# Performance work log

Hardware: AMD Instinct MI355X
Metric: run time of the kernel (lower is better)

The kernel has to match this reference:

```python
import jax, jax.numpy as jnp
import numpy as np

B, S, I, H, N_ODE = 256, 64, 256, 1024, 4


def setup_inputs() -> dict:
    key = jax.random.key(0)
    ks = jax.random.split(key, 6)
    x = jax.random.normal(ks[0], (B, S, I), dtype=jnp.float32)
    t = jnp.arange(S, dtype=jnp.float32) * 0.1  # increasing observation times
    W_in = jax.random.normal(ks[1], (H, I), dtype=jnp.float32) / np.float32(np.sqrt(I))
    b_in = jnp.zeros((H,), dtype=jnp.float32)
    W_h = jax.random.normal(ks[2], (H, H), dtype=jnp.float32) / np.float32(np.sqrt(H))
    b_h = jnp.zeros((H,), dtype=jnp.float32)
    W_ode = jax.random.normal(ks[3], (H, H), dtype=jnp.float32) / np.float32(np.sqrt(H))
    b_ode = jnp.zeros((H,), dtype=jnp.float32)
    return {"x": x, "t": t, "W_in": W_in, "b_in": b_in, "W_h": W_h,
            "b_h": b_h, "W_ode": W_ode, "b_ode": b_ode}


def reference(x, t, W_in, b_in, W_h, b_h, W_ode, b_ode):
    # x: [B, S, I], t: [S]. ODE-RNN: per timestep, evolve h by N_ODE Euler
    # steps of dh/dt = tanh(W_ode h + b_ode) over [t_{i-1}, t_i], then
    # h = tanh(W_in x_i + b_in + W_h h + b_h). First step has dt = 0
    # (original uses t[i] for both endpoints when i == 0).
    t_prev = jnp.concatenate([t[:1], t[:-1]])
    dts = t - t_prev  # [S]

    def step(h, inp):
        x_i, dt = inp  # x_i: [B, I], dt: scalar
        dth = dt / N_ODE
        def euler(hc, _):
            return hc + dth * jnp.tanh(hc @ W_ode.T + b_ode), None
        h, _ = jax.lax.scan(euler, h, None, length=N_ODE)
        h = jnp.tanh(x_i @ W_in.T + b_in + h @ W_h.T + b_h)
        return h, None

    h0 = jnp.zeros((x.shape[0], W_h.shape[0]), dtype=x.dtype)
    xs = jnp.swapaxes(x, 0, 1)  # [S, B, I]
    h_final, _ = jax.lax.scan(step, h0, (xs, dts))
    return h_final  # [B, H]
```

## Files before the change

### kernel.cpp

```cpp
#include <hip/hip_runtime.h>

#define B_ 256
#define S_ 64
#define I_ 256
#define H_ 1024
#define NODE_ 4
#define NB 256
#define NG 8
#define GSZ 32

typedef __attribute__((ext_vector_type(8))) short short8;
typedef __attribute__((ext_vector_type(4))) float f32x4;

__device__ __forceinline__ short f2bf(float f) {
    unsigned u = __float_as_uint(f);
    u += 0x7fffu + ((u >> 16) & 1u);
    return (short)(u >> 16);
}
__device__ __forceinline__ unsigned pack2(float a, float b) {
    return (unsigned)(unsigned short)f2bf(a) | ((unsigned)(unsigned short)f2bf(b) << 16);
}

__device__ __forceinline__ float ftanh(float x) {
    float e = __expf(2.0f * fabsf(x));
    float r = __builtin_fmaf(-2.0f, __builtin_amdgcn_rcpf(e + 1.0f), 1.0f);
    return copysignf(r, x);
}

__device__ __forceinline__ void gbar(unsigned* cnt, unsigned target) {
    __syncthreads();
    if (threadIdx.x == 0) {
        __hip_atomic_fetch_add(cnt, 1u, __ATOMIC_RELAXED, __HIP_MEMORY_SCOPE_AGENT);
        while (__hip_atomic_load(cnt, __ATOMIC_RELAXED, __HIP_MEMORY_SCOPE_AGENT) < target)
            __builtin_amdgcn_s_sleep(1);
    }
    __syncthreads();
}

__global__ __launch_bounds__(256, 1)
void odernn_persist(const float* __restrict__ x, const float* __restrict__ t,
                    const float* __restrict__ W_in, const float* __restrict__ b_in,
                    const float* __restrict__ W_h, const float* __restrict__ b_h,
                    const float* __restrict__ W_ode, const float* __restrict__ b_ode,
                    float* __restrict__ out,
                    unsigned short* __restrict__ h0buf, unsigned short* __restrict__ h1buf,
                    unsigned short* __restrict__ Whbf, unsigned short* __restrict__ Winbf,
                    unsigned* __restrict__ cnts)
{
    __shared__ short Wlds[32 * 1024];
    __shared__ short Hlds[32 * 1024];

    const int tid = threadIdx.x;
    const int blk = blockIdx.x;
    const int bi = blk & 7;
    const int bj = blk >> 3;
    const int lane = tid & 63;
    const int wv = tid >> 6;
    const int wr = wv >> 1, wc = wv & 1;
    const int r16 = lane & 15, kg = lane >> 4;

    {
        const int g = blk * 256 + tid;
        const float* src = W_h + (size_t)g * 16;
        unsigned* dst = (unsigned*)Whbf + (size_t)g * 8;
#pragma unroll
        for (int i = 0; i < 4; ++i) {
            float4 v = *(const float4*)(src + i * 4);
            __hip_atomic_store(dst + i * 2,     pack2(v.x, v.y), __ATOMIC_RELAXED, __HIP_MEMORY_SCOPE_AGENT);
            __hip_atomic_store(dst + i * 2 + 1, pack2(v.z, v.w), __ATOMIC_RELAXED, __HIP_MEMORY_SCOPE_AGENT);
        }
        float4 v = *(const float4*)(W_in + (size_t)g * 4);
        unsigned* d2 = (unsigned*)Winbf + (size_t)g * 2;
        __hip_atomic_store(d2,     pack2(v.x, v.y), __ATOMIC_RELAXED, __HIP_MEMORY_SCOPE_AGENT);
        __hip_atomic_store(d2 + 1, pack2(v.z, v.w), __ATOMIC_RELAXED, __HIP_MEMORY_SCOPE_AGENT);
    }

    {
        const int c = tid >> 3;
        const int ks = (tid & 7) * 128;
        const float* wsrc = W_ode + (size_t)(bj * 32 + c) * H_ + ks;
        for (int i = 0; i < 16; ++i) {
            float4 v0 = *(const float4*)(wsrc + i * 8);
            float4 v1 = *(const float4*)(wsrc + i * 8 + 4);
            short8 sv = { f2bf(v0.x), f2bf(v0.y), f2bf(v0.z), f2bf(v0.w),
                          f2bf(v1.x), f2bf(v1.y), f2bf(v1.z), f2bf(v1.w) };
            int idx = c * 1024 + ks + i * 8;
            *(short8*)&Wlds[idx ^ ((c & 7) << 3)] = sv;
        }
    }

    const int rowb = bi * 32 + wr * 16 + kg * 4;
    const int arow = bi * 32 + wr * 16 + r16;
    const int col  = bj * 32 + wc * 16 + r16;
    const int wb   = wc * 16 + r16;

    const int hrow = wr * 16 + r16;
    const char* aBase = (const char*)Hlds + hrow * 2048;
    const int hswz = (hrow & 7) << 4;

    const float bodec = b_ode[col];
    const float binc  = b_in[col] + b_h[col];

    f32x4 hreg = {0.f, 0.f, 0.f, 0.f};
#pragma unroll
    for (int r = 0; r < 4; ++r)
        __hip_atomic_store(&h0buf[(size_t)(rowb + r) * H_ + col], (unsigned short)0,
                           __ATOMIC_RELAXED, __HIP_MEMORY_SCOPE_AGENT);

    gbar(cnts + NG * 64, NB);

    unsigned* gc = cnts + bi * 64;
    unsigned tar = GSZ;

    const unsigned short* hin = h0buf;
    unsigned short* hout = h1buf;

    auto stage = [&](const unsigned short* hsrc) {
        const unsigned long long* src =
            (const unsigned long long*)(hsrc + (size_t)bi * 32 * H_);
        unsigned long long v[32];
#pragma unroll
        for (int i = 0; i < 32; ++i)
            v[i] = __hip_atomic_load(src + i * 256 + tid,
                                     __ATOMIC_RELAXED, __HIP_MEMORY_SCOPE_AGENT);
#pragma unroll
        for (int i = 0; i < 32; ++i) {
            int byte = i * 2048 + (((tid * 8) & 2047) ^ ((i & 7) << 4));
            *(unsigned long long*)((char*)Hlds + byte) = v[i];
        }
        __syncthreads();
    };

    for (int s = 0; s < S_; ++s) {
        if (s > 0) {
            const float dth = (t[s] - t[s - 1]) * 0.25f;
            for (int e = 0; e < NODE_; ++e) {
                stage(hin);
                f32x4 acc = {0.f, 0.f, 0.f, 0.f};
#pragma unroll
                for (int k0 = 0; k0 < H_; k0 += 32) {
                    short8 a = *(const short8*)(aBase + (((k0 + kg * 8) * 2) ^ hswz));
                    short8 b = *(const short8*)&Wlds[(wb * 1024 + k0 + kg * 8) ^ ((wb & 7) << 3)];
                    acc = __builtin_amdgcn_mfma_f32_16x16x32_bf16(a, b, acc, 0, 0, 0);
                }
#pragma unroll
                for (int r = 0; r < 4; ++r) {
                    hreg[r] += dth * ftanh(acc[r] + bodec);
                    __hip_atomic_store(&hout[(size_t)(rowb + r) * H_ + col],
                                       (unsigned short)f2bf(hreg[r]),
                                       __ATOMIC_RELAXED, __HIP_MEMORY_SCOPE_AGENT);
                }
                gbar(gc, tar); tar += GSZ;
                const unsigned short* tmp = hin; hin = hout; hout = (unsigned short*)tmp;
            }
        }
        {
            stage(hin);
            f32x4 acc = {0.f, 0.f, 0.f, 0.f};
            const unsigned short* whB = Whbf + (size_t)col * H_ + kg * 8;
#pragma unroll 8
            for (int k0 = 0; k0 < H_; k0 += 32) {
                short8 a = *(const short8*)(aBase + (((k0 + kg * 8) * 2) ^ hswz));
                short8 b = *(const short8*)(whB + k0);
                acc = __builtin_amdgcn_mfma_f32_16x16x32_bf16(a, b, acc, 0, 0, 0);
            }
            const float* xB = x + ((size_t)arow * S_ + s) * I_ + kg * 8;
            const unsigned short* wiB = Winbf + (size_t)col * I_ + kg * 8;
#pragma unroll
            for (int k2 = 0; k2 < I_; k2 += 32) {
                float4 a0 = *(const float4*)(xB + k2);
                float4 a1 = *(const float4*)(xB + k2 + 4);
                short8 a = { f2bf(a0.x), f2bf(a0.y), f2bf(a0.z), f2bf(a0.w),
                             f2bf(a1.x), f2bf(a1.y), f2bf(a1.z), f2bf(a1.w) };
                short8 b = *(const short8*)(wiB + k2);
                acc = __builtin_amdgcn_mfma_f32_16x16x32_bf16(a, b, acc, 0, 0, 0);
            }
            const bool last = (s == S_ - 1);
#pragma unroll
            for (int r = 0; r < 4; ++r) {
                float v = ftanh(acc[r] + binc);
                hreg[r] = v;
                if (last) {
                    out[(size_t)(rowb + r) * H_ + col] = v;
                } else {
                    __hip_atomic_store(&hout[(size_t)(rowb + r) * H_ + col],
                                       (unsigned short)f2bf(v),
                                       __ATOMIC_RELAXED, __HIP_MEMORY_SCOPE_AGENT);
                }
            }
            if (!last) {
                gbar(gc, tar); tar += GSZ;
                const unsigned short* tmp = hin; hin = hout; hout = (unsigned short*)tmp;
            }
        }
    }
}

extern "C" void kernel_launch(void* const* d_in, const int* in_sizes, int n_in,
                              void* d_out, int out_size, void* d_ws, size_t ws_size,
                              hipStream_t stream) {
    const float* x     = (const float*)d_in[0];
    const float* t     = (const float*)d_in[1];
    const float* W_in  = (const float*)d_in[2];
    const float* b_in  = (const float*)d_in[3];
    const float* W_h   = (const float*)d_in[4];
    const float* b_h   = (const float*)d_in[5];
    const float* W_ode = (const float*)d_in[6];
    const float* b_ode = (const float*)d_in[7];

    unsigned short* h0    = (unsigned short*)d_ws;
    unsigned short* h1    = h0 + (size_t)B_ * H_;
    unsigned short* Whbf  = h1 + (size_t)B_ * H_;
    unsigned short* Winbf = Whbf + (size_t)H_ * H_;
    unsigned* cnts = (unsigned*)(Winbf + (size_t)H_ * I_);

    (void)hipMemsetAsync(cnts, 0, (NG * 64 + 1) * sizeof(unsigned), stream);

    odernn_persist<<<dim3(NB), dim3(256), 0, stream>>>(
        x, t, W_in, b_in, W_h, b_h, W_ode, b_ode,
        (float*)d_out, h0, h1, Whbf, Winbf, cnts);
}
```

Before: 1.345 ms.

## Use XCC-local barriers and coalesced plain loads when a group shares an XCD

Each block reads its XCC id from a hardware register and records per-group min and max ids. When every block in a group runs on the same XCD, the group uses a device-local (non-coherent-scope) atomic counter polled with buffer_inv, plain vectorized 16-byte loads for staging h, and plain stores. Publishing h now goes through LDS so each thread writes contiguous 8-byte chunks instead of scattered 2-byte atomic stores. This aims to cut the cross-die coherence and latency cost of the per-step group barrier and h exchange, but it relies on XCD placement and L2-local atomics behaving as assumed, and it adds extra syncthreads per step.

```diff
diff --git a/kernel.cpp b/kernel.cpp
--- a/kernel.cpp
+++ b/kernel.cpp
@@ -27,12 +27,48 @@
     return copysignf(r, x);
 }
 
-__device__ __forceinline__ void gbar(unsigned* cnt, unsigned target) {
+__device__ __forceinline__ unsigned get_xcc() {
+    unsigned x;
+    asm volatile("s_getreg_b32 %0, hwreg(20, 0, 32)" : "=s"(x));
+    return x & 0xfu;
+}
+
+__device__ __forceinline__ void gbar_slow(unsigned* cnt, unsigned target) {
     __syncthreads();
     if (threadIdx.x == 0) {
         __hip_atomic_fetch_add(cnt, 1u, __ATOMIC_RELAXED, __HIP_MEMORY_SCOPE_AGENT);
         while (__hip_atomic_load(cnt, __ATOMIC_RELAXED, __HIP_MEMORY_SCOPE_AGENT) < target)
             __builtin_amdgcn_s_sleep(1);
+    }
+    __syncthreads();
+}
+
+__device__ __forceinline__ void gbar2(unsigned* gcl, unsigned* gca, unsigned target, bool fast) {
+    __syncthreads();
+    if (threadIdx.x == 0) {
+        if (fast) {
+            unsigned one = 1;
+            asm volatile("global_atomic_add %0, %1, off" :: "v"(gcl), "v"(one) : "memory");
+            __hip_atomic_fetch_add(gca, 1u, __ATOMIC_RELAXED, __HIP_MEMORY_SCOPE_AGENT);
+            unsigned v; unsigned it = 0;
+            for (;;) {
+                asm volatile("buffer_inv\n\t"
+                             "s_waitcnt vmcnt(0)\n\t"
+                             "global_load_dword %0, %1, off\n\t"
+                             "s_waitcnt vmcnt(0)"
+                             : "=&v"(v) : "v"(gcl) : "memory");
+                if (v >= target) break;
+                if ((++it & 15u) == 0 &&
+                    __hip_atomic_load(gca, __ATOMIC_RELAXED, __HIP_MEMORY_SCOPE_AGENT) >= target)
+                    break;
+                __builtin_amdgcn_s_sleep(1);
+            }
+            asm volatile("buffer_inv\n\ts_waitcnt vmcnt(0)" ::: "memory");
+        } else {
+            __hip_atomic_fetch_add(gca, 1u, __ATOMIC_RELAXED, __HIP_MEMORY_SCOPE_AGENT);
+            while (__hip_atomic_load(gca, __ATOMIC_RELAXED, __HIP_MEMORY_SCOPE_AGENT) < target)
+                __builtin_amdgcn_s_sleep(1);
+        }
     }
     __syncthreads();
 }
@@ -88,6 +124,24 @@
             *(short8*)&Wlds[idx ^ ((c & 7) << 3)] = sv;
         }
     }
+    __syncthreads();
+
+    if (tid == 0) {
+        asm volatile("buffer_inv sc1\n\ts_waitcnt vmcnt(0)" ::: "memory");
+        unsigned xc = get_xcc();
+        __hip_atomic_fetch_max(&cnts[516 + bi], xc, __ATOMIC_RELAXED, __HIP_MEMORY_SCOPE_AGENT);
+        __hip_atomic_fetch_max(&cnts[524],      xc, __ATOMIC_RELAXED, __HIP_MEMORY_SCOPE_AGENT);
+        __hip_atomic_fetch_min(&cnts[525 + bi], xc, __ATOMIC_RELAXED, __HIP_MEMORY_SCOPE_AGENT);
+        __hip_atomic_fetch_min(&cnts[533],      xc, __ATOMIC_RELAXED, __HIP_MEMORY_SCOPE_AGENT);
+    }
+
+    gbar_slow(&cnts[512], NB);
+
+    const bool fast =
+        (__hip_atomic_load(&cnts[524], __ATOMIC_RELAXED, __HIP_MEMORY_SCOPE_AGENT) !=
+         __hip_atomic_load(&cnts[533], __ATOMIC_RELAXED, __HIP_MEMORY_SCOPE_AGENT)) &&
+        (__hip_atomic_load(&cnts[516 + bi], __ATOMIC_RELAXED, __HIP_MEMORY_SCOPE_AGENT) ==
+         __hip_atomic_load(&cnts[525 + bi], __ATOMIC_RELAXED, __HIP_MEMORY_SCOPE_AGENT));
 
     const int rowb = bi * 32 + wr * 16 + kg * 4;
     const int arow = bi * 32 + wr * 16 + r16;
@@ -107,28 +161,55 @@
         __hip_atomic_store(&h0buf[(size_t)(rowb + r) * H_ + col], (unsigned short)0,
                            __ATOMIC_RELAXED, __HIP_MEMORY_SCOPE_AGENT);
 
-    gbar(cnts + NG * 64, NB);
-
-    unsigned* gc = cnts + bi * 64;
+    unsigned* gca = cnts + bi * 64;
+    unsigned* gcl = cnts + bi * 64 + 32;
     unsigned tar = GSZ;
+
+    gbar2(gcl, gca, tar, fast); tar += GSZ;
 
     const unsigned short* hin = h0buf;
     unsigned short* hout = h1buf;
 
     auto stage = [&](const unsigned short* hsrc) {
-        const unsigned long long* src =
-            (const unsigned long long*)(hsrc + (size_t)bi * 32 * H_);
-        unsigned long long v[32];
-#pragma unroll
-        for (int i = 0; i < 32; ++i)
-            v[i] = __hip_atomic_load(src + i * 256 + tid,
-                                     __ATOMIC_RELAXED, __HIP_MEMORY_SCOPE_AGENT);
-#pragma unroll
-        for (int i = 0; i < 32; ++i) {
-            int byte = i * 2048 + (((tid * 8) & 2047) ^ ((i & 7) << 4));
-            *(unsigned long long*)((char*)Hlds + byte) = v[i];
+        if (fast) {
+            const char* sp = (const char*)(hsrc + (size_t)bi * 32 * H_);
+#pragma unroll
+            for (int i = 0; i < 16; ++i) {
+                f32x4 v = *(const f32x4*)(sp + i * 4096 + tid * 16);
+                int off = i * 4096 + tid * 16;
+                int row = off >> 11, c = off & 2047;
+                *(f32x4*)((char*)Hlds + row * 2048 + (c ^ ((row & 7) << 4))) = v;
+            }
+        } else {
+            const unsigned long long* src =
+                (const unsigned long long*)(hsrc + (size_t)bi * 32 * H_);
+            unsigned long long v[32];
+#pragma unroll
+            for (int i = 0; i < 32; ++i)
+                v[i] = __hip_atomic_load(src + i * 256 + tid,
+                                         __ATOMIC_RELAXED, __HIP_MEMORY_SCOPE_AGENT);
+#pragma unroll
+            for (int i = 0; i < 32; ++i) {
+                int byte = i * 2048 + (((tid * 8) & 2047) ^ ((i & 7) << 4));
+                *(unsigned long long*)((char*)Hlds + byte) = v[i];
+            }
         }
         __syncthreads();
+    };
+
+    auto publish = [&](unsigned short* dst, f32x4 pv) {
+        __syncthreads();
+        short* Hp = (short*)Hlds;
+#pragma unroll
+        for (int r = 0; r < 4; ++r)
+            Hp[(wr * 16 + kg * 4 + r) * 32 + wc * 16 + r16] = f2bf(pv[r]);
+        __syncthreads();
+        const int row = tid >> 3, cg = tid & 7;
+        unsigned long long v = *(unsigned long long*)&Hp[row * 32 + cg * 4];
+        unsigned long long* d =
+            (unsigned long long*)&dst[(size_t)(bi * 32 + row) * H_ + bj * 32 + cg * 4];
+        if (fast) *d = v;
+        else __hip_atomic_store(d, v, __ATOMIC_RELAXED, __HIP_MEMORY_SCOPE_AGENT);
     };
 
     for (int s = 0; s < S_; ++s) {
@@ -144,13 +225,10 @@
                     acc = __builtin_amdgcn_mfma_f32_16x16x32_bf16(a, b, acc, 0, 0, 0);
                 }
 #pragma unroll
-                for (int r = 0; r < 4; ++r) {
+                for (int r = 0; r < 4; ++r)
                     hreg[r] += dth * ftanh(acc[r] + bodec);
-                    __hip_atomic_store(&hout[(size_t)(rowb + r) * H_ + col],
-                                       (unsigned short)f2bf(hreg[r]),
-                                       __ATOMIC_RELAXED, __HIP_MEMORY_SCOPE_AGENT);
-                }
-                gbar(gc, tar); tar += GSZ;
+                publish(hout, hreg);
+                gbar2(gcl, gca, tar, fast); tar += GSZ;
                 const unsigned short* tmp = hin; hin = hout; hout = (unsigned short*)tmp;
             }
         }
@@ -176,23 +254,27 @@
                 acc = __builtin_amdgcn_mfma_f32_16x16x32_bf16(a, b, acc, 0, 0, 0);
             }
             const bool last = (s == S_ - 1);
+            f32x4 hv;
 #pragma unroll
             for (int r = 0; r < 4; ++r) {
-                float v = ftanh(acc[r] + binc);
-                hreg[r] = v;
-                if (last) {
-                    out[(size_t)(rowb + r) * H_ + col] = v;
-                } else {
-                    __hip_atomic_store(&hout[(size_t)(rowb + r) * H_ + col],
-                                       (unsigned short)f2bf(v),
-                                       __ATOMIC_RELAXED, __HIP_MEMORY_SCOPE_AGENT);
-                }
-            }
-            if (!last) {
-                gbar(gc, tar); tar += GSZ;
+                hv[r] = ftanh(acc[r] + binc);
+                hreg[r] = hv[r];
+            }
+            if (last) {
+#pragma unroll
+                for (int r = 0; r < 4; ++r)
+                    out[(size_t)(rowb + r) * H_ + col] = hv[r];
+            } else {
+                publish(hout, hv);
+                gbar2(gcl, gca, tar, fast); tar += GSZ;
                 const unsigned short* tmp = hin; hin = hout; hout = (unsigned short*)tmp;
             }
         }
+    }
+
+    if (fast && tid == 0 && bj == 0) {
+        unsigned fin = tar - GSZ;
+        asm volatile("global_atomic_sub %0, %1, off" :: "v"(gcl), "v"(fin) : "memory");
     }
 }
 
@@ -214,7 +296,8 @@
     unsigned short* Winbf = Whbf + (size_t)H_ * H_;
     unsigned* cnts = (unsigned*)(Winbf + (size_t)H_ * I_);
 
-    (void)hipMemsetAsync(cnts, 0, (NG * 64 + 1) * sizeof(unsigned), stream);
+    (void)hipMemsetAsync(cnts, 0, 525 * sizeof(unsigned), stream);
+    (void)hipMemsetAsync(cnts + 525, 0xFF, 9 * sizeof(unsigned), stream);
 
     odernn_persist<<<dim3(NB), dim3(256), 0, stream>>>(
         x, t, W_in, b_in, W_h, b_h, W_ode, b_ode,
```

Result: slower. 1.971 ms (+46.5%).

## Replace group counter barrier with per-block epoch flags and overlap staging with MFMA

Applied to the files above, without the earlier changes.

The shared atomic counter barrier for each 32-block group becomes per-block epoch flags, polled by one wave across the group with __all. Hidden-state outputs are first gathered through LDS and then published as 64-bit stores. Staging of the h tile is split into halves so the second half's global loads overlap MFMA work on the first half. The reductions use two accumulators to break the MFMA dependency chain. This adds extra __syncthreads per step and a more involved flag protocol that relies on the s_waitcnt ordering being correct.

```diff
diff --git a/kernel.cpp b/kernel.cpp
--- a/kernel.cpp
+++ b/kernel.cpp
@@ -27,7 +27,7 @@
     return copysignf(r, x);
 }
 
-__device__ __forceinline__ void gbar(unsigned* cnt, unsigned target) {
+__device__ __forceinline__ void gbar_slow(unsigned* cnt, unsigned target) {
     __syncthreads();
     if (threadIdx.x == 0) {
         __hip_atomic_fetch_add(cnt, 1u, __ATOMIC_RELAXED, __HIP_MEMORY_SCOPE_AGENT);
@@ -107,89 +107,152 @@
         __hip_atomic_store(&h0buf[(size_t)(rowb + r) * H_ + col], (unsigned short)0,
                            __ATOMIC_RELAXED, __HIP_MEMORY_SCOPE_AGENT);
 
-    gbar(cnts + NG * 64, NB);
-
-    unsigned* gc = cnts + bi * 64;
-    unsigned tar = GSZ;
+    gbar_slow(&cnts[512], NB);
+
+    unsigned* flags = cnts + 1024 + bi * 32;
+    unsigned ep = 1;
+
+    const int srow = tid >> 3, scl = tid & 7;
+    const int swz_w = (srow & 7) << 4;
+
+    auto stage_issue_half = [&](const unsigned short* hsrc, int half, unsigned long long* v) {
+        const unsigned long long* src =
+            (const unsigned long long*)(hsrc + (size_t)bi * 32 * H_) +
+            srow * 256 + half * 128 + scl;
+#pragma unroll
+        for (int j = 0; j < 16; ++j)
+            v[j] = __hip_atomic_load(src + j * 8, __ATOMIC_RELAXED, __HIP_MEMORY_SCOPE_AGENT);
+    };
+    auto stage_write_half = [&](int half, const unsigned long long* v) {
+#pragma unroll
+        for (int j = 0; j < 16; ++j) {
+            int inb = half * 1024 + j * 64 + scl * 8;
+            *(unsigned long long*)((char*)Hlds + srow * 2048 + (inb ^ swz_w)) = v[j];
+        }
+    };
+
+    auto mfma_half_lds = [&](int base, f32x4& acc0, f32x4& acc1) {
+#pragma unroll
+        for (int k0 = base; k0 < base + 512; k0 += 64) {
+            short8 a0 = *(const short8*)(aBase + (((k0 + kg * 8) * 2) ^ hswz));
+            short8 b0 = *(const short8*)&Wlds[(wb * 1024 + k0 + kg * 8) ^ ((wb & 7) << 3)];
+            acc0 = __builtin_amdgcn_mfma_f32_16x16x32_bf16(a0, b0, acc0, 0, 0, 0);
+            short8 a1 = *(const short8*)(aBase + (((k0 + 32 + kg * 8) * 2) ^ hswz));
+            short8 b1 = *(const short8*)&Wlds[(wb * 1024 + k0 + 32 + kg * 8) ^ ((wb & 7) << 3)];
+            acc1 = __builtin_amdgcn_mfma_f32_16x16x32_bf16(a1, b1, acc1, 0, 0, 0);
+        }
+    };
+    auto mfma_half_glb = [&](int base, const unsigned short* whB, f32x4& acc0, f32x4& acc1) {
+#pragma unroll
+        for (int k0 = base; k0 < base + 512; k0 += 64) {
+            short8 a0 = *(const short8*)(aBase + (((k0 + kg * 8) * 2) ^ hswz));
+            short8 b0 = *(const short8*)(whB + k0);
+            acc0 = __builtin_amdgcn_mfma_f32_16x16x32_bf16(a0, b0, acc0, 0, 0, 0);
+            short8 a1 = *(const short8*)(aBase + (((k0 + 32 + kg * 8) * 2) ^ hswz));
+            short8 b1 = *(const short8*)(whB + k0 + 32);
+            acc1 = __builtin_amdgcn_mfma_f32_16x16x32_bf16(a1, b1, acc1, 0, 0, 0);
+        }
+    };
+
+    auto publish_barrier = [&](unsigned short* dst, f32x4 pv, unsigned epoch) {
+        __syncthreads();
+        short* Hp = (short*)Hlds;
+#pragma unroll
+        for (int r = 0; r < 4; ++r)
+            Hp[(wr * 16 + kg * 4 + r) * 32 + wc * 16 + r16] = f2bf(pv[r]);
+        __syncthreads();
+        if (wv == 0) {
+#pragma unroll
+            for (int j = 0; j < 4; ++j) {
+                int idx = j * 64 + lane;
+                int row = idx >> 3, cg = idx & 7;
+                unsigned long long vv = *(unsigned long long*)&Hp[row * 32 + cg * 4];
+                __hip_atomic_store(
+                    (unsigned long long*)&dst[(size_t)(bi * 32 + row) * H_ + bj * 32 + cg * 4],
+                    vv, __ATOMIC_RELAXED, __HIP_MEMORY_SCOPE_AGENT);
+            }
+            asm volatile("s_waitcnt vmcnt(0)" ::: "memory");
+            if (lane == 0)
+                __hip_atomic_store(&flags[bj], epoch, __ATOMIC_RELAXED, __HIP_MEMORY_SCOPE_AGENT);
+            const unsigned* fp = flags + (lane & 31);
+            for (;;) {
+                unsigned v = __hip_atomic_load(fp, __ATOMIC_RELAXED, __HIP_MEMORY_SCOPE_AGENT);
+                if (__all((int)(v >= epoch))) break;
+                __builtin_amdgcn_s_sleep(1);
+            }
+        }
+        __syncthreads();
+    };
 
     const unsigned short* hin = h0buf;
     unsigned short* hout = h1buf;
-
-    auto stage = [&](const unsigned short* hsrc) {
-        const unsigned long long* src =
-            (const unsigned long long*)(hsrc + (size_t)bi * 32 * H_);
-        unsigned long long v[32];
-#pragma unroll
-        for (int i = 0; i < 32; ++i)
-            v[i] = __hip_atomic_load(src + i * 256 + tid,
-                                     __ATOMIC_RELAXED, __HIP_MEMORY_SCOPE_AGENT);
-#pragma unroll
-        for (int i = 0; i < 32; ++i) {
-            int byte = i * 2048 + (((tid * 8) & 2047) ^ ((i & 7) << 4));
-            *(unsigned long long*)((char*)Hlds + byte) = v[i];
-        }
-        __syncthreads();
-    };
 
     for (int s = 0; s < S_; ++s) {
         if (s > 0) {
             const float dth = (t[s] - t[s - 1]) * 0.25f;
             for (int e = 0; e < NODE_; ++e) {
-                stage(hin);
-                f32x4 acc = {0.f, 0.f, 0.f, 0.f};
-#pragma unroll
-                for (int k0 = 0; k0 < H_; k0 += 32) {
-                    short8 a = *(const short8*)(aBase + (((k0 + kg * 8) * 2) ^ hswz));
-                    short8 b = *(const short8*)&Wlds[(wb * 1024 + k0 + kg * 8) ^ ((wb & 7) << 3)];
-                    acc = __builtin_amdgcn_mfma_f32_16x16x32_bf16(a, b, acc, 0, 0, 0);
-                }
-#pragma unroll
-                for (int r = 0; r < 4; ++r) {
+                unsigned long long vA[16], vB[16];
+                stage_issue_half(hin, 0, vA);
+                stage_write_half(0, vA);
+                stage_issue_half(hin, 1, vB);
+                __syncthreads();
+                f32x4 acc0 = {0.f, 0.f, 0.f, 0.f}, acc1 = {0.f, 0.f, 0.f, 0.f};
+                mfma_half_lds(0, acc0, acc1);
+                stage_write_half(1, vB);
+                __syncthreads();
+                mfma_half_lds(512, acc0, acc1);
+                f32x4 acc = acc0 + acc1;
+#pragma unroll
+                for (int r = 0; r < 4; ++r)
                     hreg[r] += dth * ftanh(acc[r] + bodec);
-                    __hip_atomic_store(&hout[(size_t)(rowb + r) * H_ + col],
-                                       (unsigned short)f2bf(hreg[r]),
-                                       __ATOMIC_RELAXED, __HIP_MEMORY_SCOPE_AGENT);
-                }
-                gbar(gc, tar); tar += GSZ;
+                publish_barrier(hout, hreg, ep); ++ep;
                 const unsigned short* tmp = hin; hin = hout; hout = (unsigned short*)tmp;
             }
         }
         {
-            stage(hin);
-            f32x4 acc = {0.f, 0.f, 0.f, 0.f};
             const unsigned short* whB = Whbf + (size_t)col * H_ + kg * 8;
-#pragma unroll 8
-            for (int k0 = 0; k0 < H_; k0 += 32) {
-                short8 a = *(const short8*)(aBase + (((k0 + kg * 8) * 2) ^ hswz));
-                short8 b = *(const short8*)(whB + k0);
-                acc = __builtin_amdgcn_mfma_f32_16x16x32_bf16(a, b, acc, 0, 0, 0);
-            }
+            unsigned long long vA[16], vB[16];
+            stage_issue_half(hin, 0, vA);
+            stage_write_half(0, vA);
+            stage_issue_half(hin, 1, vB);
+            __syncthreads();
+            f32x4 acc0 = {0.f, 0.f, 0.f, 0.f}, acc1 = {0.f, 0.f, 0.f, 0.f};
+            mfma_half_glb(0, whB, acc0, acc1);
+            stage_write_half(1, vB);
+            __syncthreads();
+            mfma_half_glb(512, whB, acc0, acc1);
+
             const float* xB = x + ((size_t)arow * S_ + s) * I_ + kg * 8;
             const unsigned short* wiB = Winbf + (size_t)col * I_ + kg * 8;
 #pragma unroll
-            for (int k2 = 0; k2 < I_; k2 += 32) {
-                float4 a0 = *(const float4*)(xB + k2);
-                float4 a1 = *(const float4*)(xB + k2 + 4);
-                short8 a = { f2bf(a0.x), f2bf(a0.y), f2bf(a0.z), f2bf(a0.w),
-                             f2bf(a1.x), f2bf(a1.y), f2bf(a1.z), f2bf(a1.w) };
+            for (int k2 = 0; k2 < I_; k2 += 64) {
+                float4 a0f = *(const float4*)(xB + k2);
+                float4 a1f = *(const float4*)(xB + k2 + 4);
+                short8 a = { f2bf(a0f.x), f2bf(a0f.y), f2bf(a0f.z), f2bf(a0f.w),
+                             f2bf(a1f.x), f2bf(a1f.y), f2bf(a1f.z), f2bf(a1f.w) };
                 short8 b = *(const short8*)(wiB + k2);
-                acc = __builtin_amdgcn_mfma_f32_16x16x32_bf16(a, b, acc, 0, 0, 0);
-            }
+                acc0 = __builtin_amdgcn_mfma_f32_16x16x32_bf16(a, b, acc0, 0, 0, 0);
+                float4 a2f = *(const float4*)(xB + k2 + 32);
+                float4 a3f = *(const float4*)(xB + k2 + 36);
+                short8 a2 = { f2bf(a2f.x), f2bf(a2f.y), f2bf(a2f.z), f2bf(a2f.w),
+                              f2bf(a3f.x), f2bf(a3f.y), f2bf(a3f.z), f2bf(a3f.w) };
+                short8 b2 = *(const short8*)(wiB + k2 + 32);
+                acc1 = __builtin_amdgcn_mfma_f32_16x16x32_bf16(a2, b2, acc1, 0, 0, 0);
+            }
+            f32x4 acc = acc0 + acc1;
             const bool last = (s == S_ - 1);
+            f32x4 hv;
 #pragma unroll
             for (int r = 0; r < 4; ++r) {
-                float v = ftanh(acc[r] + binc);
-                hreg[r] = v;
-                if (last) {
-                    out[(size_t)(rowb + r) * H_ + col] = v;
-                } else {
-                    __hip_atomic_store(&hout[(size_t)(rowb + r) * H_ + col],
-                                       (unsigned short)f2bf(v),
-                                       __ATOMIC_RELAXED, __HIP_MEMORY_SCOPE_AGENT);
-                }
-            }
-            if (!last) {
-                gbar(gc, tar); tar += GSZ;
+                hv[r] = ftanh(acc[r] + binc);
+                hreg[r] = hv[r];
+            }
+            if (last) {
+#pragma unroll
+                for (int r = 0; r < 4; ++r)
+                    out[(size_t)(rowb + r) * H_ + col] = hv[r];
+            } else {
+                publish_barrier(hout, hv, ep); ++ep;
                 const unsigned short* tmp = hin; hin = hout; hout = (unsigned short*)tmp;
             }
         }
@@ -214,7 +277,7 @@
     unsigned short* Winbf = Whbf + (size_t)H_ * H_;
     unsigned* cnts = (unsigned*)(Winbf + (size_t)H_ * I_);
 
-    (void)hipMemsetAsync(cnts, 0, (NG * 64 + 1) * sizeof(unsigned), stream);
+    (void)hipMemsetAsync(cnts, 0, (1024 + NG * GSZ) * sizeof(unsigned), stream);
 
     odernn_persist<<<dim3(NB), dim3(256), 0, stream>>>(
         x, t, W_in, b_in, W_h, b_h, W_ode, b_ode,
```

Result: slower. 1.624 ms (+20.7%).
